# Kernel optimization log

Measured on AMD Instinct MI355X. Metric: run time of the kernel, lower is better.

Reference implementation:

```python
import jax, jax.numpy as jnp
import numpy as np

B, N, NPOINT, NSAMPLE = 8, 16384, 512, 64
RADIUS = 0.1
C_IN = 64
DIMS = [64, 64, 128]


def setup_inputs() -> dict:
    key = jax.random.key(0)
    ks = jax.random.split(key, 8)
    xyz = jax.random.uniform(ks[0], (B, N, 3), jnp.float32)          # points in unit cube
    features = jax.random.normal(ks[1], (B, C_IN, N), jnp.float32)   # (B, C, N) per GroupGatherByIndex
    dims = [3 + C_IN] + DIMS                                         # use_xyz_feature adds 3
    out = {"xyz": xyz, "features": features}
    for i in range(3):
        out[f"W{i+1}"] = jax.random.normal(ks[2 + i], (dims[i], dims[i + 1]), jnp.float32) / np.sqrt(dims[i])
        out[f"b{i+1}"] = jnp.zeros((dims[i + 1],), jnp.float32)
    return out


def furthest_point_sampling(xyz, npoint):
    # Iterative FPS starting at index 0 (matches CUDA kernel semantics).
    Bq, Nq, _ = xyz.shape
    barange = jnp.arange(Bq)

    def step(carry, _):
        dists, last = carry
        p = xyz[barange, last]                       # (B, 3)
        d = jnp.sum((xyz - p[:, None, :]) ** 2, -1)  # (B, N)
        dists = jnp.minimum(dists, d)
        nxt = jnp.argmax(dists, axis=1).astype(jnp.int32)
        return (dists, nxt), nxt

    init = (jnp.full((Bq, Nq), 1e10, xyz.dtype), jnp.zeros((Bq,), jnp.int32))
    _, idxs = jax.lax.scan(step, init, None, length=npoint - 1)
    return jnp.concatenate([jnp.zeros((Bq, 1), jnp.int32), idxs.T], axis=1)  # (B, npoint)


def ball_query(new_xyz, xyz, radius, nsample):
    # For each centroid, first nsample in-ball indices (ascending), padded with first hit.
    Nq = xyz.shape[1]
    d2 = jnp.sum((new_xyz[:, :, None, :] - xyz[:, None, :, :]) ** 2, -1)  # (B, npoint, N)
    cand = jnp.where(d2 < radius * radius, jnp.arange(Nq, dtype=jnp.int32), Nq)
    cand = jnp.sort(cand, axis=-1)[..., :nsample]                          # (B, npoint, nsample)
    first = jnp.where(cand[..., :1] == Nq, 0, cand[..., :1])
    return jnp.where(cand == Nq, first, cand)


def reference(xyz, features, W1, b1, W2, b2, W3, b3):
    fps_idx = furthest_point_sampling(xyz, NPOINT)                  # (B, npoint)
    new_xyz = jax.vmap(lambda p, i: p[i])(xyz, fps_idx)             # (B, npoint, 3)
    idx = ball_query(new_xyz, xyz, RADIUS, NSAMPLE)                 # (B, npoint, nsample)
    grouped_xyz = jax.vmap(lambda p, i: p[i])(xyz, idx)             # (B, npoint, nsample, 3)
    centered = grouped_xyz - new_xyz[:, :, None, :]                 # centroid subtract
    feats_n = jnp.transpose(features, (0, 2, 1))                    # (B, N, C)
    grouped_f = jax.vmap(lambda f, i: f[i])(feats_n, idx)           # (B, npoint, nsample, C)
    h = jnp.concatenate([centered, grouped_f], axis=-1)             # (B, npoint, nsample, 3+C)
    for W, b in ((W1, b1), (W2, b2), (W3, b3)):                     # pointwise 1x1-conv MLP + ReLU
        h = jax.nn.relu(h @ W + b)
    return jnp.max(h, axis=2)                                       # max-pool over nsample -> (B, npoint, C_out)
```

## Files before the change

kernel.cpp:

```cpp
#include <hip/hip_runtime.h>

#define NB 8
#define NPTS 16384
#define NPOINT 512
#define NSAMPLE 64
#define CIN 64

typedef float v2f __attribute__((ext_vector_type(2)));

__device__ __forceinline__ v2f pk_add(v2f a, v2f b) {
    v2f d;
    asm("v_pk_add_f32 %0, %1, %2" : "=v"(d) : "v"(a), "v"(b));
    return d;
}
__device__ __forceinline__ v2f pk_mul(v2f a, v2f b) {
    v2f d;
    asm("v_pk_mul_f32 %0, %1, %2" : "=v"(d) : "v"(a), "v"(b));
    return d;
}

template <int CTRL>
__device__ __forceinline__ float dpp_f(float x) {
    int xi = __builtin_bit_cast(int, x);
    int yi = __builtin_amdgcn_update_dpp(xi, xi, CTRL, 0xF, 0xF, false);
    return __builtin_bit_cast(float, yi);
}
template <int CTRL>
__device__ __forceinline__ int dpp_i(int x) {
    return __builtin_amdgcn_update_dpp(x, x, CTRL, 0xF, 0xF, false);
}

__device__ __forceinline__ float wave_max_f(float x) {
    x = fmaxf(x, dpp_f<0x111>(x));
    x = fmaxf(x, dpp_f<0x112>(x));
    x = fmaxf(x, dpp_f<0x114>(x));
    x = fmaxf(x, dpp_f<0x118>(x));
    x = fmaxf(x, dpp_f<0x142>(x));
    x = fmaxf(x, dpp_f<0x143>(x));
    return x;
}
__device__ __forceinline__ int wave_min_i(int x) {
    x = min(x, dpp_i<0x111>(x));
    x = min(x, dpp_i<0x112>(x));
    x = min(x, dpp_i<0x114>(x));
    x = min(x, dpp_i<0x118>(x));
    x = min(x, dpp_i<0x142>(x));
    x = min(x, dpp_i<0x143>(x));
    return x;
}

#define CMB(va, ia, vb, ib) { bool t_ = ((vb) > (va)) || (((vb) == (va)) && ((ib) < (ia))); \
                              if (t_) { (va) = (vb); (ia) = (ib); } }

__global__ __launch_bounds__(512, 1) void fps_transpose_kernel(
    const float* __restrict__ xyz, const float* __restrict__ feats,
    int* __restrict__ fps_idx, float* __restrict__ feats_t)
{
    __shared__ float t[64][65];
    __shared__ __align__(16) int s_pair[2][8][2];

    if (blockIdx.x >= NB) {
        int blk = blockIdx.x - NB;
        int b = blk & 7;
        int tile = blk >> 3;
        int n0 = tile * 64;
        int cc = threadIdx.x & 63, rr = threadIdx.x >> 6;
        const float* fb = feats + (size_t)b * CIN * NPTS;
        #pragma unroll
        for (int k = 0; k < 8; ++k) {
            int c = rr + k * 8;
            t[c][cc] = fb[(size_t)c * NPTS + n0 + cc];
        }
        __syncthreads();
        float* fo = feats_t + ((size_t)b * NPTS + n0) * CIN;
        #pragma unroll
        for (int k = 0; k < 8; ++k) {
            int n = rr + k * 8;
            fo[n * CIN + cc] = t[cc][n];
        }
        return;
    }

    const int b = blockIdx.x;
    const int tid = threadIdx.x;
    const int wv = tid >> 6, ln = tid & 63;
    const float* xb = xyz + (size_t)b * NPTS * 3;
    const int base = tid * 32;

    v2f px2[16], py2[16], pz2[16];
    float dd[32];
    {
        const float4* xb4 = (const float4*)(xb + (size_t)base * 3);
        #pragma unroll
        for (int q = 0; q < 8; ++q) {
            float4 f0 = xb4[3 * q + 0];
            float4 f1 = xb4[3 * q + 1];
            float4 f2 = xb4[3 * q + 2];
            px2[2 * q + 0] = (v2f){f0.x, f0.w};
            py2[2 * q + 0] = (v2f){f0.y, f1.x};
            pz2[2 * q + 0] = (v2f){f0.z, f1.y};
            px2[2 * q + 1] = (v2f){f1.z, f2.y};
            py2[2 * q + 1] = (v2f){f1.w, f2.z};
            pz2[2 * q + 1] = (v2f){f2.x, f2.w};
        }
        #pragma unroll
        for (int k = 0; k < 32; ++k) dd[k] = 1e10f;
    }
    if (tid == 0) fps_idx[b * NPOINT] = 0;
    float cx = xb[0], cy = xb[1], cz = xb[2];
    __syncthreads();

    for (int j = 1; j < NPOINT; ++j) {
        const int p = j & 1;
        v2f ncx = (v2f){-cx, -cx};
        v2f ncy = (v2f){-cy, -cy};
        v2f ncz = (v2f){-cz, -cz};
        float bm = -1.0f;
        #pragma unroll
        for (int k = 0; k < 16; ++k) {
            v2f dx = pk_add(px2[k], ncx);
            v2f dy = pk_add(py2[k], ncy);
            v2f dz = pk_add(pz2[k], ncz);
            v2f sx = pk_mul(dx, dx);
            v2f sy = pk_mul(dy, dy);
            v2f sz = pk_mul(dz, dz);
            v2f s1 = pk_add(sx, sy);
            v2f d2 = pk_add(s1, sz);
            float n0 = fminf(dd[2 * k + 0], d2.x);
            float n1 = fminf(dd[2 * k + 1], d2.y);
            dd[2 * k + 0] = n0;
            dd[2 * k + 1] = n1;
            bm = fmaxf(fmaxf(bm, n0), n1);
        }
        float wm = wave_max_f(bm);
        float wmax = __builtin_bit_cast(float,
            __builtin_amdgcn_readlane(__builtin_bit_cast(int, wm), 63));
        int mi = 0x7fffffff;
        #pragma unroll
        for (int k = 31; k >= 0; --k)
            mi = (dd[k] == wmax) ? (base + k) : mi;
        int rm = wave_min_i(mi);
        int wave_mi = __builtin_amdgcn_readlane(rm, 63);
        if (ln == 0) {
            s_pair[p][wv][0] = __builtin_bit_cast(int, wmax);
            s_pair[p][wv][1] = wave_mi;
        }
        __syncthreads();
        int4 q0 = *(const int4*)&s_pair[p][0][0];
        int4 q1 = *(const int4*)&s_pair[p][2][0];
        int4 q2 = *(const int4*)&s_pair[p][4][0];
        int4 q3 = *(const int4*)&s_pair[p][6][0];
        float v0 = __builtin_bit_cast(float, q0.x); int i0 = q0.y;
        float v1 = __builtin_bit_cast(float, q0.z); int i1 = q0.w;
        float v2 = __builtin_bit_cast(float, q1.x); int i2 = q1.y;
        float v3 = __builtin_bit_cast(float, q1.z); int i3 = q1.w;
        float v4 = __builtin_bit_cast(float, q2.x); int i4 = q2.y;
        float v5 = __builtin_bit_cast(float, q2.z); int i5 = q2.w;
        float v6 = __builtin_bit_cast(float, q3.x); int i6 = q3.y;
        float v7 = __builtin_bit_cast(float, q3.z); int i7 = q3.w;
        CMB(v0, i0, v1, i1); CMB(v2, i2, v3, i3);
        CMB(v4, i4, v5, i5); CMB(v6, i6, v7, i7);
        CMB(v0, i0, v2, i2); CMB(v4, i4, v6, i6);
        CMB(v0, i0, v4, i4);
        int ch = __builtin_amdgcn_readfirstlane(i0);
        const float* cp = xb + 3 * ch;
        cx = cp[0]; cy = cp[1]; cz = cp[2];
        if (tid == 0) fps_idx[b * NPOINT + j] = ch;
    }
}

__global__ __launch_bounds__(64) void ball_kernel(
    const float* __restrict__ xyz, const int* __restrict__ fps_idx, int* __restrict__ ball_idx)
{
    const float R2 = (float)(0.1 * 0.1);
    int blk = blockIdx.x;
    int b = blk & 7, j = blk >> 3;
    int lane = threadIdx.x;
    int cent = b * NPOINT + j;
    const float* xb = xyz + (size_t)b * NPTS * 3;
    int cidx = fps_idx[cent];
    float cx = xb[3 * cidx + 0];
    float cy = xb[3 * cidx + 1];
    float cz = xb[3 * cidx + 2];

    __shared__ int slots[64];
    int cnt = 0;
    for (int base = 0; base < NPTS; base += 64) {
        int i = base + lane;
        float dx = __fsub_rn(xb[3 * i + 0], cx);
        float dy = __fsub_rn(xb[3 * i + 1], cy);
        float dz = __fsub_rn(xb[3 * i + 2], cz);
        float d2 = __fadd_rn(__fadd_rn(__fmul_rn(dx, dx), __fmul_rn(dy, dy)), __fmul_rn(dz, dz));
        bool inb = d2 < R2;
        unsigned long long m = __ballot(inb);
        int pre = (int)__popcll(m & ((1ull << lane) - 1ull));
        int slot = cnt + pre;
        if (inb && slot < NSAMPLE) slots[slot] = i;
        cnt += (int)__popcll(m);
        if (cnt >= NSAMPLE) break;
    }
    __syncthreads();
    int first = (cnt > 0) ? slots[0] : 0;
    int v = (lane < cnt) ? slots[lane] : first;
    ball_idx[(size_t)cent * NSAMPLE + lane] = v;
}

__global__ __launch_bounds__(64) void mlp_kernel(
    const float* __restrict__ xyz, const float* __restrict__ feats_t,
    const int* __restrict__ fps_idx, const int* __restrict__ ball_idx,
    const float* __restrict__ W1, const float* __restrict__ b1,
    const float* __restrict__ W2, const float* __restrict__ b2,
    const float* __restrict__ W3, const float* __restrict__ b3,
    float* __restrict__ out)
{
    int blk = blockIdx.x;
    int b = blk & 7, j = blk >> 3;
    int s = threadIdx.x;
    int cent = b * NPOINT + j;

    __shared__ float X[64][68];

    int i = ball_idx[(size_t)cent * NSAMPLE + s];
    int cidx = fps_idx[cent];
    const float* cp = xyz + ((size_t)b * NPTS + cidx) * 3;
    float cx = cp[0], cy = cp[1], cz = cp[2];
    const float* pp = xyz + ((size_t)b * NPTS + i) * 3;
    X[s][64] = pp[0] - cx;
    X[s][65] = pp[1] - cy;
    X[s][66] = pp[2] - cz;
    const float4* fr = (const float4*)(feats_t + ((size_t)b * NPTS + i) * CIN);
    #pragma unroll
    for (int q = 0; q < 16; ++q) *(float4*)&X[s][q * 4] = fr[q];

    float acc[64];
    #pragma unroll
    for (int o = 0; o < 64; ++o) acc[o] = b1[o];
    for (int c = 0; c < 67; ++c) {
        float xc = X[s][c];
        const float* w = W1 + ((c < 64) ? (c + 3) : (c - 64)) * 64;
        #pragma unroll
        for (int o = 0; o < 64; ++o) acc[o] = fmaf(xc, w[o], acc[o]);
    }
    #pragma unroll
    for (int o = 0; o < 64; ++o) X[s][o] = fmaxf(acc[o], 0.0f);

    #pragma unroll
    for (int o = 0; o < 64; ++o) acc[o] = b2[o];
    for (int c = 0; c < 64; ++c) {
        float xc = X[s][c];
        const float* w = W2 + c * 64;
        #pragma unroll
        for (int o = 0; o < 64; ++o) acc[o] = fmaf(xc, w[o], acc[o]);
    }
    #pragma unroll
    for (int o = 0; o < 64; ++o) X[s][o] = fmaxf(acc[o], 0.0f);

    float h3[128];
    #pragma unroll
    for (int o = 0; o < 128; ++o) h3[o] = b3[o];
    for (int c = 0; c < 64; ++c) {
        float xc = X[s][c];
        const float* w = W3 + c * 128;
        #pragma unroll
        for (int o = 0; o < 128; ++o) h3[o] = fmaf(xc, w[o], h3[o]);
    }

    #pragma unroll
    for (int o = 0; o < 128; ++o) {
        float v = fmaxf(h3[o], 0.0f);
        #pragma unroll
        for (int off = 1; off < 64; off <<= 1) v = fmaxf(v, __shfl_xor(v, off));
        h3[o] = v;
    }
    if (s == 0) {
        float* op = out + (size_t)cent * 128;
        #pragma unroll
        for (int o = 0; o < 128; o += 4) {
            float4 v = make_float4(h3[o], h3[o + 1], h3[o + 2], h3[o + 3]);
            *(float4*)&op[o] = v;
        }
    }
}

extern "C" void kernel_launch(void* const* d_in, const int* in_sizes, int n_in,
                              void* d_out, int out_size, void* d_ws, size_t ws_size,
                              hipStream_t stream) {
    const float* xyz   = (const float*)d_in[0];
    const float* feats = (const float*)d_in[1];
    const float* W1 = (const float*)d_in[2];
    const float* b1 = (const float*)d_in[3];
    const float* W2 = (const float*)d_in[4];
    const float* b2 = (const float*)d_in[5];
    const float* W3 = (const float*)d_in[6];
    const float* b3 = (const float*)d_in[7];
    float* out = (float*)d_out;

    char* ws = (char*)d_ws;
    int*   fps_idx  = (int*)ws;
    int*   ball_idx = (int*)(ws + 16384);
    float* feats_t  = (float*)(ws + 16384 + 1048576);

    fps_transpose_kernel<<<NB + NB * (NPTS / 64), 512, 0, stream>>>(xyz, feats, fps_idx, feats_t);
    ball_kernel<<<NB * NPOINT, 64, 0, stream>>>(xyz, fps_idx, ball_idx);
    mlp_kernel<<<NB * NPOINT, 64, 0, stream>>>(xyz, feats_t, fps_idx, ball_idx,
                                               W1, b1, W2, b2, W3, b3, out);
}
```

Measured before the change: 1.244 ms.

## Widen FPS block to 1024 threads, DPP final reduce, transpose MLP shared tile

The FPS kernel now runs 1024 threads per batch with 16 points per thread instead of 32. This halves the serial per-thread distance work in each of the 511 iterations, at the cost of 16 wave partials per step. The cross-wave argmax is now a DPP lane reduction over the 16 partials rather than a scalar compare tree, and the transpose blocks are adjusted to the larger block size. The MLP kernel's shared tile becomes channel-major, so per-sample reads and writes hit consecutive banks instead of a padded row-per-thread layout.

```diff
diff --git a/kernel.cpp b/kernel.cpp
--- a/kernel.cpp
+++ b/kernel.cpp
@@ -5,6 +5,7 @@
 #define NPOINT 512
 #define NSAMPLE 64
 #define CIN 64
+#define PPT 16
 
 typedef float v2f __attribute__((ext_vector_type(2)));
 
@@ -49,15 +50,12 @@
     return x;
 }
 
-#define CMB(va, ia, vb, ib) { bool t_ = ((vb) > (va)) || (((vb) == (va)) && ((ib) < (ia))); \
-                              if (t_) { (va) = (vb); (ia) = (ib); } }
-
-__global__ __launch_bounds__(512, 1) void fps_transpose_kernel(
+__global__ __launch_bounds__(1024, 4) void fps_transpose_kernel(
     const float* __restrict__ xyz, const float* __restrict__ feats,
     int* __restrict__ fps_idx, float* __restrict__ feats_t)
 {
     __shared__ float t[64][65];
-    __shared__ __align__(16) int s_pair[2][8][2];
+    __shared__ __align__(16) int s_pair[2][16][2];
 
     if (blockIdx.x >= NB) {
         int blk = blockIdx.x - NB;
@@ -67,15 +65,15 @@
         int cc = threadIdx.x & 63, rr = threadIdx.x >> 6;
         const float* fb = feats + (size_t)b * CIN * NPTS;
         #pragma unroll
-        for (int k = 0; k < 8; ++k) {
-            int c = rr + k * 8;
+        for (int k = 0; k < 4; ++k) {
+            int c = rr + k * 16;
             t[c][cc] = fb[(size_t)c * NPTS + n0 + cc];
         }
         __syncthreads();
         float* fo = feats_t + ((size_t)b * NPTS + n0) * CIN;
         #pragma unroll
-        for (int k = 0; k < 8; ++k) {
-            int n = rr + k * 8;
+        for (int k = 0; k < 4; ++k) {
+            int n = rr + k * 16;
             fo[n * CIN + cc] = t[cc][n];
         }
         return;
@@ -85,14 +83,14 @@
     const int tid = threadIdx.x;
     const int wv = tid >> 6, ln = tid & 63;
     const float* xb = xyz + (size_t)b * NPTS * 3;
-    const int base = tid * 32;
-
-    v2f px2[16], py2[16], pz2[16];
-    float dd[32];
+    const int base = tid * PPT;
+
+    v2f px2[8], py2[8], pz2[8];
+    float dd[16];
     {
         const float4* xb4 = (const float4*)(xb + (size_t)base * 3);
         #pragma unroll
-        for (int q = 0; q < 8; ++q) {
+        for (int q = 0; q < 4; ++q) {
             float4 f0 = xb4[3 * q + 0];
             float4 f1 = xb4[3 * q + 1];
             float4 f2 = xb4[3 * q + 2];
@@ -104,7 +102,7 @@
             pz2[2 * q + 1] = (v2f){f2.x, f2.w};
         }
         #pragma unroll
-        for (int k = 0; k < 32; ++k) dd[k] = 1e10f;
+        for (int k = 0; k < 16; ++k) dd[k] = 1e10f;
     }
     if (tid == 0) fps_idx[b * NPOINT] = 0;
     float cx = xb[0], cy = xb[1], cz = xb[2];
@@ -117,7 +115,7 @@
         v2f ncz = (v2f){-cz, -cz};
         float bm = -1.0f;
         #pragma unroll
-        for (int k = 0; k < 16; ++k) {
+        for (int k = 0; k < 8; ++k) {
             v2f dx = pk_add(px2[k], ncx);
             v2f dy = pk_add(py2[k], ncy);
             v2f dz = pk_add(pz2[k], ncz);
@@ -137,7 +135,7 @@
             __builtin_amdgcn_readlane(__builtin_bit_cast(int, wm), 63));
         int mi = 0x7fffffff;
         #pragma unroll
-        for (int k = 31; k >= 0; --k)
+        for (int k = PPT - 1; k >= 0; --k)
             mi = (dd[k] == wmax) ? (base + k) : mi;
         int rm = wave_min_i(mi);
         int wave_mi = __builtin_amdgcn_readlane(rm, 63);
@@ -146,23 +144,21 @@
             s_pair[p][wv][1] = wave_mi;
         }
         __syncthreads();
-        int4 q0 = *(const int4*)&s_pair[p][0][0];
-        int4 q1 = *(const int4*)&s_pair[p][2][0];
-        int4 q2 = *(const int4*)&s_pair[p][4][0];
-        int4 q3 = *(const int4*)&s_pair[p][6][0];
-        float v0 = __builtin_bit_cast(float, q0.x); int i0 = q0.y;
-        float v1 = __builtin_bit_cast(float, q0.z); int i1 = q0.w;
-        float v2 = __builtin_bit_cast(float, q1.x); int i2 = q1.y;
-        float v3 = __builtin_bit_cast(float, q1.z); int i3 = q1.w;
-        float v4 = __builtin_bit_cast(float, q2.x); int i4 = q2.y;
-        float v5 = __builtin_bit_cast(float, q2.z); int i5 = q2.w;
-        float v6 = __builtin_bit_cast(float, q3.x); int i6 = q3.y;
-        float v7 = __builtin_bit_cast(float, q3.z); int i7 = q3.w;
-        CMB(v0, i0, v1, i1); CMB(v2, i2, v3, i3);
-        CMB(v4, i4, v5, i5); CMB(v6, i6, v7, i7);
-        CMB(v0, i0, v2, i2); CMB(v4, i4, v6, i6);
-        CMB(v0, i0, v4, i4);
-        int ch = __builtin_amdgcn_readfirstlane(i0);
+        int2 pr = *(const int2*)&s_pair[p][ln & 15][0];
+        float v = __builtin_bit_cast(float, pr.x);
+        int   i = pr.y;
+        {
+            float ov; int oi; bool tk;
+            ov = dpp_f<0x111>(v); oi = dpp_i<0x111>(i);
+            tk = (ov > v) || (ov == v && oi < i); v = tk ? ov : v; i = tk ? oi : i;
+            ov = dpp_f<0x112>(v); oi = dpp_i<0x112>(i);
+            tk = (ov > v) || (ov == v && oi < i); v = tk ? ov : v; i = tk ? oi : i;
+            ov = dpp_f<0x114>(v); oi = dpp_i<0x114>(i);
+            tk = (ov > v) || (ov == v && oi < i); v = tk ? ov : v; i = tk ? oi : i;
+            ov = dpp_f<0x118>(v); oi = dpp_i<0x118>(i);
+            tk = (ov > v) || (ov == v && oi < i); v = tk ? ov : v; i = tk ? oi : i;
+        }
+        int ch = __builtin_amdgcn_readlane(i, 15);
         const float* cp = xb + 3 * ch;
         cx = cp[0]; cy = cp[1]; cz = cp[2];
         if (tid == 0) fps_idx[b * NPOINT + j] = ch;
@@ -218,48 +214,54 @@
     int s = threadIdx.x;
     int cent = b * NPOINT + j;
 
-    __shared__ float X[64][68];
+    __shared__ float X[67][64];
 
     int i = ball_idx[(size_t)cent * NSAMPLE + s];
     int cidx = fps_idx[cent];
     const float* cp = xyz + ((size_t)b * NPTS + cidx) * 3;
     float cx = cp[0], cy = cp[1], cz = cp[2];
     const float* pp = xyz + ((size_t)b * NPTS + i) * 3;
-    X[s][64] = pp[0] - cx;
-    X[s][65] = pp[1] - cy;
-    X[s][66] = pp[2] - cz;
+    X[64][s] = pp[0] - cx;
+    X[65][s] = pp[1] - cy;
+    X[66][s] = pp[2] - cz;
     const float4* fr = (const float4*)(feats_t + ((size_t)b * NPTS + i) * CIN);
     #pragma unroll
-    for (int q = 0; q < 16; ++q) *(float4*)&X[s][q * 4] = fr[q];
+    for (int q = 0; q < 16; ++q) {
+        float4 f = fr[q];
+        X[q * 4 + 0][s] = f.x;
+        X[q * 4 + 1][s] = f.y;
+        X[q * 4 + 2][s] = f.z;
+        X[q * 4 + 3][s] = f.w;
+    }
 
     float acc[64];
     #pragma unroll
     for (int o = 0; o < 64; ++o) acc[o] = b1[o];
     for (int c = 0; c < 67; ++c) {
-        float xc = X[s][c];
+        float xc = X[c][s];
         const float* w = W1 + ((c < 64) ? (c + 3) : (c - 64)) * 64;
         #pragma unroll
         for (int o = 0; o < 64; ++o) acc[o] = fmaf(xc, w[o], acc[o]);
     }
     #pragma unroll
-    for (int o = 0; o < 64; ++o) X[s][o] = fmaxf(acc[o], 0.0f);
+    for (int o = 0; o < 64; ++o) X[o][s] = fmaxf(acc[o], 0.0f);
 
     #pragma unroll
     for (int o = 0; o < 64; ++o) acc[o] = b2[o];
     for (int c = 0; c < 64; ++c) {
-        float xc = X[s][c];
+        float xc = X[c][s];
         const float* w = W2 + c * 64;
         #pragma unroll
         for (int o = 0; o < 64; ++o) acc[o] = fmaf(xc, w[o], acc[o]);
     }
     #pragma unroll
-    for (int o = 0; o < 64; ++o) X[s][o] = fmaxf(acc[o], 0.0f);
+    for (int o = 0; o < 64; ++o) X[o][s] = fmaxf(acc[o], 0.0f);
 
     float h3[128];
     #pragma unroll
     for (int o = 0; o < 128; ++o) h3[o] = b3[o];
     for (int c = 0; c < 64; ++c) {
-        float xc = X[s][c];
+        float xc = X[c][s];
         const float* w = W3 + c * 128;
         #pragma unroll
         for (int o = 0; o < 128; ++o) h3[o] = fmaf(xc, w[o], h3[o]);
@@ -300,7 +302,7 @@
     int*   ball_idx = (int*)(ws + 16384);
     float* feats_t  = (float*)(ws + 16384 + 1048576);
 
-    fps_transpose_kernel<<<NB + NB * (NPTS / 64), 512, 0, stream>>>(xyz, feats, fps_idx, feats_t);
+    fps_transpose_kernel<<<NB + NB * (NPTS / 64), 1024, 0, stream>>>(xyz, feats, fps_idx, feats_t);
     ball_kernel<<<NB * NPOINT, 64, 0, stream>>>(xyz, fps_idx, ball_idx);
     mlp_kernel<<<NB * NPOINT, 64, 0, stream>>>(xyz, feats_t, fps_idx, ball_idx,
                                                W1, b1, W2, b2, W3, b3, out);
```

Result: slower. 1.325 ms (+6.5%).
